# Performance work log

Hardware: AMD Instinct MI355X
Metric: run time of the kernel (lower is better)

The kernel has to match this reference:

```python
import jax, jax.numpy as jnp
import numpy as np

B, N, K = 8, 2048, 20
CIN, COUT, DIM, PH, MULT, UP = 256, 128, 64, 64, 4, 2
EPS = 1e-5

def _lin(k, o, i):
    return jax.random.normal(k, (o, i), jnp.float32) * (1.0 / np.sqrt(i))

def setup_inputs() -> dict:
    key = jax.random.key(0)
    ks = jax.random.split(key, 32)
    H = DIM * MULT
    return {
        'pos': jax.random.normal(ks[0], (B, 3, N), jnp.float32),
        'key_feat': jax.random.normal(ks[1], (B, CIN, N), jnp.float32),
        'query_feat': jax.random.normal(ks[2], (B, CIN, N), jnp.float32),
        'upfeat': jax.random.normal(ks[3], (B, CIN, N), jnp.float32),
        'mv_w1': _lin(ks[4], CIN, 2 * CIN), 'mv_b1': jnp.zeros(CIN),
        'mv_w2': _lin(ks[5], CIN, CIN), 'mv_b2': jnp.zeros(CIN),
        'mv_ws': _lin(ks[6], CIN, 2 * CIN), 'mv_bs': jnp.zeros(CIN),
        'wk': _lin(ks[7], DIM, CIN), 'bk': jnp.zeros(DIM),
        'wq': _lin(ks[8], DIM, CIN), 'bq': jnp.zeros(DIM),
        'wv': _lin(ks[9], DIM, CIN), 'bv': jnp.zeros(DIM),
        'wu': _lin(ks[10], DIM, CIN), 'bu': jnp.zeros(DIM),
        'pm_w1': _lin(ks[11], PH, 3), 'pm_b1': jnp.zeros(PH),
        'pm_g': jnp.ones(PH) + 0.1 * jax.random.normal(ks[12], (PH,)),
        'pm_be': 0.1 * jax.random.normal(ks[13], (PH,)),
        'pm_m': 0.1 * jax.random.normal(ks[14], (PH,)),
        'pm_v': jax.random.uniform(ks[15], (PH,), minval=0.5, maxval=1.5),
        'pm_w2': _lin(ks[16], DIM, PH), 'pm_b2': jnp.zeros(DIM),
        'am_w1': _lin(ks[17], H, DIM), 'am_b1': jnp.zeros(H),
        'am_g': jnp.ones(H) + 0.1 * jax.random.normal(ks[18], (H,)),
        'am_be': 0.1 * jax.random.normal(ks[19], (H,)),
        'am_m': 0.1 * jax.random.normal(ks[20], (H,)),
        'am_v': jax.random.uniform(ks[21], (H,), minval=0.5, maxval=1.5),
        'am_wt': jax.random.normal(ks[22], (H, DIM, UP), jnp.float32) * (1.0 / np.sqrt(H)),
        'am_bt': jnp.zeros(DIM),
        'we': _lin(ks[23], COUT, DIM), 'be': jnp.zeros(COUT),
        'wr': _lin(ks[24], COUT, CIN), 'br': jnp.zeros(COUT),
    }

def _c1(x, w, b):  # 1x1 Conv1d: x (B,C,N)
    return jnp.einsum('oc,bcn->bon', w, x) + b[None, :, None]

def _c2(x, w, b):  # 1x1 Conv2d: x (B,C,N,K)
    return jnp.einsum('oc,bcnk->bonk', w, x) + b[None, :, None, None]

def _bn(x, g, be, m, v):  # eval-mode BatchNorm2d over channel dim
    sc = g / jnp.sqrt(v + EPS)
    return x * sc[None, :, None, None] + (be - m * sc)[None, :, None, None]

def _group(f, idx):  # f (B,C,N), idx (B,N,K) -> (B,C,N,K)
    return jax.vmap(lambda fb, ib: fb[:, ib])(f, idx)

def reference(pos, key_feat, query_feat, upfeat, mv_w1, mv_b1, mv_w2, mv_b2, mv_ws, mv_bs, wk, bk, wq, bq, wv, bv, wu, bu, pm_w1, pm_b1, pm_g, pm_be, pm_m, pm_v, pm_w2, pm_b2, am_w1, am_b1, am_g, am_be, am_m, am_v, am_wt, am_bt, we, be, wr, br):
    # mlp_v: MLP_Res(in=2*CIN, hidden=CIN, out=CIN)
    x = jnp.concatenate([key_feat, query_feat], axis=1)
    value = _c1(jax.nn.relu(_c1(x, mv_w1, mv_b1)), mv_w2, mv_b2) + _c1(x, mv_ws, mv_bs)
    identity = value
    k = _c1(key_feat, wk, bk)
    q = _c1(query_feat, wq, bq)
    v = _c1(value, wv, bv)
    # self-KNN on pos
    pt = jnp.swapaxes(pos, 1, 2)  # (B,N,3)
    sq = jnp.sum(pt * pt, -1)
    d2 = sq[:, :, None] + sq[:, None, :] - 2.0 * jnp.einsum('bnc,bmc->bnm', pt, pt)
    _, idx = jax.lax.top_k(-d2, K)  # (B,N,K)
    k_g = _group(k, idx)
    qk_rel = q[..., None] - k_g  # (B,DIM,N,K)
    pos_rel = pos[..., None] - _group(pos, idx)  # (B,3,N,K)
    pe = _c2(jax.nn.relu(_bn(_c2(pos_rel, pm_w1, pm_b1), pm_g, pm_be, pm_m, pm_v)), pm_w2, pm_b2)
    uf = _c1(upfeat, wu, bu)
    uf_rel = uf[..., None] - _group(uf, idx)
    # attn_mlp: conv2d -> BN -> ReLU -> ConvTranspose2d((UP,1),(UP,1))
    h = jax.nn.relu(_bn(_c2(qk_rel + pe + uf_rel, am_w1, am_b1), am_g, am_be, am_m, am_v))  # (B,H,N,K)
    attn = jnp.einsum('bcnk,cor->bonrk', h, am_wt)  # (B,DIM,N,UP,K)
    b_, o_, n_, r_, k_ = attn.shape
    attn = attn.reshape(b_, o_, n_ * r_, k_) + am_bt[None, :, None, None]  # (B,DIM,UP*N,K)
    attn = jax.nn.softmax(attn, axis=-1)  # scale_layer = Softmax(dim=-1)
    val = _group(v, idx) + pe + uf_rel  # (B,DIM,N,K)
    val = jnp.repeat(val, UP, axis=2)  # nearest Upsample (UP,1)
    agg = jnp.sum(attn * val, axis=-1)  # (B,DIM,UP*N)
    y = _c1(agg, we, be)
    iden = jnp.repeat(_c1(identity, wr, br), UP, axis=2)
    return y + iden
```

## Files before the change

kernel.cpp:

```cpp
#include <hip/hip_runtime.h>
#include <hip/hip_bf16.h>

constexpr int B_ = 8, N_ = 2048, K_ = 20;
constexpr float EPS_ = 1e-5f;

constexpr int OW1P = 0;
constexpr int OWSP = OW1P + 256 * 256;
constexpr int OW2P = OWSP + 256 * 256;
constexpr int OWVP = OW2P + 128 * 256;
constexpr int OWRP = OWVP + 128 * 64;
constexpr int OWQT = OWRP + 128 * 128;
constexpr int OWKT = OWQT + 256 * 64;
constexpr int OWUT = OWKT + 256 * 64;
constexpr int OWET = OWUT + 256 * 64;
constexpr int OWTF = OWET + 64 * 128;
constexpr int OAWF = OWTF + 16384;
constexpr int OPWF = OAWF + 8192;
constexpr int OPW1 = OPWF + 2048;
constexpr int OB1  = OPW1 + 192;
constexpr int OBS2 = OB1 + 256;
constexpr int OBQ  = OBS2 + 256;
constexpr int OBK  = OBQ + 64;
constexpr int OBV  = OBK + 64;
constexpr int OBU  = OBV + 64;
constexpr int OBR  = OBU + 64;
constexpr int OBE  = OBR + 128;
constexpr int OPB1 = OBE + 128;
constexpr int OPSC = OPB1 + 64;
constexpr int OPSH = OPSC + 64;
constexpr int OPB2 = OPSH + 64;
constexpr int OASC = OPB2 + 64;
constexpr int OASH = OASC + 256;
constexpr int OAB1 = OASH + 256;
constexpr int OABT = OAB1 + 256;

constexpr size_t OFFB_WF   = 0;
constexpr size_t OFFB_IDX  = (size_t)2 << 20;
constexpr size_t OFFB_Q    = (size_t)4 << 20;
constexpr size_t OFFB_K    = (size_t)8 << 20;
constexpr size_t OFFB_U    = (size_t)12 << 20;
constexpr size_t OFFB_V    = (size_t)16 << 20;
constexpr size_t OFFB_IDEN = (size_t)20 << 20;

struct InPtrs { const float* p[38]; };

typedef _Float16 half2_t __attribute__((ext_vector_type(2)));
typedef _Float16 f16x8_t __attribute__((ext_vector_type(8)));
typedef float    f32x4_t __attribute__((ext_vector_type(4)));

union U4H8 { uint4 u; f16x8_t h; };

__device__ __forceinline__ unsigned pkh2(float a, float b) {
  union { unsigned u; half2_t h; } x;
  x.h = half2_t{(_Float16)a, (_Float16)b};
  return x.u;
}
__device__ __forceinline__ f32x4_t mfma_16x16x32(f16x8_t a, f16x8_t b, f32x4_t c) {
  return __builtin_amdgcn_mfma_f32_16x16x32_f16(a, b, c, 0, 0, 0);
}

__global__ __launch_bounds__(256) void k_prep(InPtrs in, float* __restrict__ wf) {
  const int tid = blockIdx.x * 256 + threadIdx.x;
  const int nth = gridDim.x * 256;
  const float *mv_w1 = in.p[4], *mv_b1 = in.p[5], *mv_w2 = in.p[6], *mv_b2 = in.p[7],
              *mv_ws = in.p[8], *mv_bs = in.p[9], *wk = in.p[10], *bk = in.p[11],
              *wq = in.p[12], *bq = in.p[13], *wv = in.p[14], *bv = in.p[15],
              *wu = in.p[16], *bu = in.p[17], *pm_w1 = in.p[18], *pm_b1 = in.p[19],
              *pm_g = in.p[20], *pm_be = in.p[21], *pm_m = in.p[22], *pm_v = in.p[23],
              *pm_w2 = in.p[24], *pm_b2 = in.p[25], *am_w1 = in.p[26], *am_b1 = in.p[27],
              *am_g = in.p[28], *am_be = in.p[29], *am_m = in.p[30], *am_v = in.p[31],
              *am_wt = in.p[32], *am_bt = in.p[33], *we = in.p[34], *be = in.p[35],
              *wr = in.p[36], *br = in.p[37];

  {
    unsigned* w1f = (unsigned*)(wf + OW1P);
    for (int i = tid; i < 65536; i += nth) {
      int q = i & 3, l = (i >> 2) & 63, ks = (i >> 8) & 15, mt = i >> 12;
      int m = mt * 16 + (l & 15);
      int k = ks * 32 + ((l >> 4) << 3) + 2 * q;
      w1f[i] = pkh2(mv_w1[m * 512 + k], mv_w1[m * 512 + k + 1]);
    }
    unsigned* wsf = (unsigned*)(wf + OWSP);
    for (int i = tid; i < 65536; i += nth) {
      int q = i & 3, l = (i >> 2) & 63, ks = (i >> 8) & 15, mt = i >> 12;
      int m = mt * 16 + (l & 15);
      int k = ks * 32 + ((l >> 4) << 3) + 2 * q;
      wsf[i] = pkh2(mv_ws[m * 512 + k], mv_ws[m * 512 + k + 1]);
    }
    unsigned* w2f = (unsigned*)(wf + OW2P);
    for (int i = tid; i < 32768; i += nth) {
      int q = i & 3, l = (i >> 2) & 63, ks = (i >> 8) & 7, mt = i >> 11;
      int m = mt * 16 + (l & 15);
      int k = ks * 32 + ((l >> 4) << 3) + 2 * q;
      w2f[i] = pkh2(mv_w2[m * 256 + k], mv_w2[m * 256 + k + 1]);
    }
    unsigned* wvf = (unsigned*)(wf + OWVP);
    for (int i = tid; i < 8192; i += nth) {
      int q = i & 3, l = (i >> 2) & 63, ks = (i >> 8) & 7, mt = i >> 11;
      int m = mt * 16 + (l & 15);
      int k = ks * 32 + ((l >> 4) << 3) + 2 * q;
      wvf[i] = pkh2(wv[m * 256 + k], wv[m * 256 + k + 1]);
    }
    unsigned* wrf = (unsigned*)(wf + OWRP);
    for (int i = tid; i < 16384; i += nth) {
      int q = i & 3, l = (i >> 2) & 63, ks = (i >> 8) & 7, mt = i >> 11;
      int m = mt * 16 + (l & 15);
      int k = ks * 32 + ((l >> 4) << 3) + 2 * q;
      wrf[i] = pkh2(wr[m * 256 + k], wr[m * 256 + k + 1]);
    }
    unsigned* wqf = (unsigned*)(wf + OWQT);
    for (int i = tid; i < 8192; i += nth) {
      int q = i & 3, l = (i >> 2) & 63, ks = (i >> 8) & 7, mt = i >> 11;
      int m = mt * 16 + (l & 15);
      int k = ks * 32 + ((l >> 4) << 3) + 2 * q;
      wqf[i] = pkh2(wq[m * 256 + k], wq[m * 256 + k + 1]);
    }
    unsigned* wkf = (unsigned*)(wf + OWKT);
    for (int i = tid; i < 8192; i += nth) {
      int q = i & 3, l = (i >> 2) & 63, ks = (i >> 8) & 7, mt = i >> 11;
      int m = mt * 16 + (l & 15);
      int k = ks * 32 + ((l >> 4) << 3) + 2 * q;
      wkf[i] = pkh2(wk[m * 256 + k], wk[m * 256 + k + 1]);
    }
  }
  for (int i = tid; i < 256 * 64; i += nth) { int c = i >> 6, m = i & 63; wf[OWUT + i] = wu[m * 256 + c]; }
  for (int i = tid; i < 64 * 128; i += nth) { int o = i >> 7, co = i & 127; wf[OWET + i] = we[co * 64 + o]; }

  {
    unsigned* wtf = (unsigned*)(wf + OWTF);
    for (int i = tid; i < 16384; i += nth) {
      int q = i & 3, l = (i >> 2) & 63, ks = (i >> 8) & 7, mt = i >> 11;
      int orr = mt * 16 + (l & 15);
      int c = ks * 32 + ((l >> 4) << 3) + 2 * q;
      wtf[i] = pkh2(am_wt[c * 128 + orr], am_wt[(c + 1) * 128 + orr]);
    }
  }
  {
    unsigned* awf = (unsigned*)(wf + OAWF);
    for (int i = tid; i < 8192; i += nth) {
      int q = i & 3, l = (i >> 2) & 63, ks = (i >> 8) & 1, mt = i >> 9;
      int c = mt * 16 + (l & 15);
      int o = ks * 32 + ((l >> 4) << 3) + 2 * q;
      awf[i] = pkh2(am_w1[c * 64 + o], am_w1[c * 64 + o + 1]);
    }
  }
  {
    unsigned* pwf = (unsigned*)(wf + OPWF);
    for (int i = tid; i < 2048; i += nth) {
      int q = i & 3, l = (i >> 2) & 63, ks = (i >> 8) & 1, mt = i >> 9;
      int o = mt * 16 + (l & 15);
      int ph = ks * 32 + ((l >> 4) << 3) + 2 * q;
      pwf[i] = pkh2(pm_w2[o * 64 + ph], pm_w2[o * 64 + ph + 1]);
    }
  }
  for (int i = tid; i < 192; i += nth) wf[OPW1 + i] = pm_w1[i];
  for (int i = tid; i < 256; i += nth) {
    wf[OB1 + i] = mv_b1[i];
    wf[OBS2 + i] = mv_bs[i] + mv_b2[i];
    float sc = am_g[i] / sqrtf(am_v[i] + EPS_);
    wf[OASC + i] = sc;
    wf[OASH + i] = am_be[i] - am_m[i] * sc;
    wf[OAB1 + i] = am_b1[i];
  }
  for (int i = tid; i < 64; i += nth) {
    wf[OBQ + i] = bq[i]; wf[OBK + i] = bk[i];
    wf[OBV + i] = bv[i]; wf[OBU + i] = bu[i];
    wf[OABT + i] = am_bt[i]; wf[OPB1 + i] = pm_b1[i]; wf[OPB2 + i] = pm_b2[i];
    float sc = pm_g[i] / sqrtf(pm_v[i] + EPS_);
    wf[OPSC + i] = sc;
    wf[OPSH + i] = pm_be[i] - pm_m[i] * sc;
  }
  for (int i = tid; i < 128; i += nth) { wf[OBR + i] = br[i]; wf[OBE + i] = be[i]; }
}

__global__ __launch_bounds__(256, 2) void k_mv(const float* __restrict__ wf,
                                               const float* __restrict__ keyf,
                                               const float* __restrict__ qryf,
                                               float* __restrict__ vout,
                                               float* __restrict__ idenout,
                                               float* __restrict__ qout,
                                               float* __restrict__ kout) {
  const int b = blockIdx.y;
  const int n0 = blockIdx.x * 32;
  const int tid = threadIdx.x, lane = tid & 63, wid = tid >> 6;
  __shared__ __align__(16) char smem[49152];
  char* xsb = smem;
  char* hbb = smem + 32768;
  char* vbb = smem;

  {
    const int col = tid & 31, kq = tid >> 5;
    const int swz = (col & 7) << 4;
#pragma unroll 4
    for (int it = 0; it < 32; ++it) {
      int k2 = it * 8 + kq;
      int c = 2 * k2;
      const float* s = (c < 256) ? keyf : qryf;
      size_t base = ((size_t)b * 256 + (c & 255)) * N_ + n0 + col;
      float x0 = s[base], x1 = s[base + N_];
      *(unsigned*)(xsb + ((col * 1024 + k2 * 4) ^ swz)) = pkh2(x0, x1);
    }
  }
  __syncthreads();

  f32x4_t acch[4][2], accs[4][2];
#pragma unroll
  for (int m = 0; m < 4; ++m)
#pragma unroll
    for (int nt = 0; nt < 2; ++nt) {
      acch[m][nt] = f32x4_t{0.f, 0.f, 0.f, 0.f};
      accs[m][nt] = f32x4_t{0.f, 0.f, 0.f, 0.f};
    }
  {
    const uint4* w1f = (const uint4*)((const unsigned*)(wf + OW1P));
    const uint4* wsf = (const uint4*)((const unsigned*)(wf + OWSP));
#pragma unroll 2
    for (int ks = 0; ks < 16; ++ks) {
      U4H8 bu[2];
#pragma unroll
      for (int nt = 0; nt < 2; ++nt) {
        int col = nt * 16 + (lane & 15);
        bu[nt].u = *(const uint4*)(xsb + ((col * 1024 + ks * 64 + ((lane >> 4) << 4)) ^ ((col & 7) << 4)));
      }
#pragma unroll
      for (int m = 0; m < 4; ++m) {
        U4H8 a1, as_;
        a1.u = w1f[((wid * 4 + m) * 16 + ks) * 64 + lane];
        as_.u = wsf[((wid * 4 + m) * 16 + ks) * 64 + lane];
#pragma unroll
        for (int nt = 0; nt < 2; ++nt) {
          acch[m][nt] = mfma_16x16x32(a1.h, bu[nt].h, acch[m][nt]);
          accs[m][nt] = mfma_16x16x32(as_.h, bu[nt].h, accs[m][nt]);
        }
      }
    }
  }
#pragma unroll
  for (int m = 0; m < 4; ++m) {
    int ch0 = (wid * 4 + m) * 16 + ((lane >> 4) << 2);
    float4 b1v = *(const float4*)(wf + OB1 + ch0);
#pragma unroll
    for (int nt = 0; nt < 2; ++nt) {
      int col = nt * 16 + (lane & 15);
      float h0 = fmaxf(acch[m][nt][0] + b1v.x, 0.f);
      float h1 = fmaxf(acch[m][nt][1] + b1v.y, 0.f);
      float h2 = fmaxf(acch[m][nt][2] + b1v.z, 0.f);
      float h3 = fmaxf(acch[m][nt][3] + b1v.w, 0.f);
      uint2 p;
      p.x = pkh2(h0, h1);
      p.y = pkh2(h2, h3);
      *(uint2*)(hbb + ((col * 512 + ch0 * 2) ^ ((col & 7) << 4))) = p;
    }
  }

  {
    f32x4_t accq[2], acck[2];
#pragma unroll
    for (int nt = 0; nt < 2; ++nt) {
      accq[nt] = f32x4_t{0.f, 0.f, 0.f, 0.f};
      acck[nt] = f32x4_t{0.f, 0.f, 0.f, 0.f};
    }
    const uint4* wqf = (const uint4*)((const unsigned*)(wf + OWQT));
    const uint4* wkf = (const uint4*)((const unsigned*)(wf + OWKT));
#pragma unroll 2
    for (int ks8 = 0; ks8 < 8; ++ks8) {
      U4H8 bk_[2], bq_[2];
#pragma unroll
      for (int nt = 0; nt < 2; ++nt) {
        int col = nt * 16 + (lane & 15);
        int swz = (col & 7) << 4;
        bk_[nt].u = *(const uint4*)(xsb + ((col * 1024 + ks8 * 64 + ((lane >> 4) << 4)) ^ swz));
        bq_[nt].u = *(const uint4*)(xsb + ((col * 1024 + (8 + ks8) * 64 + ((lane >> 4) << 4)) ^ swz));
      }
      U4H8 aq, ak;
      aq.u = wqf[(wid * 8 + ks8) * 64 + lane];
      ak.u = wkf[(wid * 8 + ks8) * 64 + lane];
#pragma unroll
      for (int nt = 0; nt < 2; ++nt) {
        acck[nt] = mfma_16x16x32(ak.h, bk_[nt].h, acck[nt]);
        accq[nt] = mfma_16x16x32(aq.h, bq_[nt].h, accq[nt]);
      }
    }
    int ch0 = wid * 16 + ((lane >> 4) << 2);
    float4 bqv = *(const float4*)(wf + OBQ + ch0);
    float4 bkv = *(const float4*)(wf + OBK + ch0);
#pragma unroll
    for (int nt = 0; nt < 2; ++nt) {
      int col = nt * 16 + (lane & 15);
      *(float4*)(qout + ((size_t)b * N_ + n0 + col) * 64 + ch0) =
          make_float4(accq[nt][0] + bqv.x, accq[nt][1] + bqv.y,
                      accq[nt][2] + bqv.z, accq[nt][3] + bqv.w);
      *(float4*)(kout + ((size_t)b * N_ + n0 + col) * 64 + ch0) =
          make_float4(acck[nt][0] + bkv.x, acck[nt][1] + bkv.y,
                      acck[nt][2] + bkv.z, acck[nt][3] + bkv.w);
    }
  }
  __syncthreads();

  {
    f32x4_t acc2[4][2];
#pragma unroll
    for (int m = 0; m < 4; ++m)
#pragma unroll
      for (int nt = 0; nt < 2; ++nt) acc2[m][nt] = f32x4_t{0.f, 0.f, 0.f, 0.f};
    const uint4* w2f = (const uint4*)((const unsigned*)(wf + OW2P));
#pragma unroll 2
    for (int ks = 0; ks < 8; ++ks) {
      U4H8 bu[2];
#pragma unroll
      for (int nt = 0; nt < 2; ++nt) {
        int col = nt * 16 + (lane & 15);
        bu[nt].u = *(const uint4*)(hbb + ((col * 512 + ks * 64 + ((lane >> 4) << 4)) ^ ((col & 7) << 4)));
      }
#pragma unroll
      for (int m = 0; m < 4; ++m) {
        U4H8 a2;
        a2.u = w2f[((wid * 4 + m) * 8 + ks) * 64 + lane];
#pragma unroll
        for (int nt = 0; nt < 2; ++nt)
          acc2[m][nt] = mfma_16x16x32(a2.h, bu[nt].h, acc2[m][nt]);
      }
    }
#pragma unroll
    for (int m = 0; m < 4; ++m) {
      int ch0 = (wid * 4 + m) * 16 + ((lane >> 4) << 2);
      float4 bsv = *(const float4*)(wf + OBS2 + ch0);
#pragma unroll
      for (int nt = 0; nt < 2; ++nt) {
        int col = nt * 16 + (lane & 15);
        float v0 = acc2[m][nt][0] + accs[m][nt][0] + bsv.x;
        float v1 = acc2[m][nt][1] + accs[m][nt][1] + bsv.y;
        float v2 = acc2[m][nt][2] + accs[m][nt][2] + bsv.z;
        float v3 = acc2[m][nt][3] + accs[m][nt][3] + bsv.w;
        uint2 p;
        p.x = pkh2(v0, v1);
        p.y = pkh2(v2, v3);
        *(uint2*)(vbb + ((col * 512 + ch0 * 2) ^ ((col & 7) << 4))) = p;
      }
    }
  }
  __syncthreads();

  {
    f32x4_t accv[2], accr[2][2];
#pragma unroll
    for (int nt = 0; nt < 2; ++nt) {
      accv[nt] = f32x4_t{0.f, 0.f, 0.f, 0.f};
      accr[0][nt] = f32x4_t{0.f, 0.f, 0.f, 0.f};
      accr[1][nt] = f32x4_t{0.f, 0.f, 0.f, 0.f};
    }
    const uint4* wvf = (const uint4*)((const unsigned*)(wf + OWVP));
    const uint4* wrf = (const uint4*)((const unsigned*)(wf + OWRP));
#pragma unroll 2
    for (int ks = 0; ks < 8; ++ks) {
      U4H8 bu[2];
#pragma unroll
      for (int nt = 0; nt < 2; ++nt) {
        int col = nt * 16 + (lane & 15);
        bu[nt].u = *(const uint4*)(vbb + ((col * 512 + ks * 64 + ((lane >> 4) << 4)) ^ ((col & 7) << 4)));
      }
      U4H8 av;
      av.u = wvf[(wid * 8 + ks) * 64 + lane];
#pragma unroll
      for (int nt = 0; nt < 2; ++nt)
        accv[nt] = mfma_16x16x32(av.h, bu[nt].h, accv[nt]);
#pragma unroll
      for (int m2 = 0; m2 < 2; ++m2) {
        U4H8 ar;
        ar.u = wrf[((wid * 2 + m2) * 8 + ks) * 64 + lane];
#pragma unroll
        for (int nt = 0; nt < 2; ++nt)
          accr[m2][nt] = mfma_16x16x32(ar.h, bu[nt].h, accr[m2][nt]);
      }
    }
    {
      int ch0 = wid * 16 + ((lane >> 4) << 2);
      float4 bvv = *(const float4*)(wf + OBV + ch0);
#pragma unroll
      for (int nt = 0; nt < 2; ++nt) {
        int col = nt * 16 + (lane & 15);
        *(float4*)(vout + ((size_t)b * N_ + n0 + col) * 64 + ch0) =
            make_float4(accv[nt][0] + bvv.x, accv[nt][1] + bvv.y,
                        accv[nt][2] + bvv.z, accv[nt][3] + bvv.w);
      }
    }
#pragma unroll
    for (int m2 = 0; m2 < 2; ++m2) {
      int ch0 = (wid * 2 + m2) * 16 + ((lane >> 4) << 2);
      float4 brv = *(const float4*)(wf + OBR + ch0);
#pragma unroll
      for (int nt = 0; nt < 2; ++nt) {
        int col = nt * 16 + (lane & 15);
        *(float4*)(idenout + ((size_t)b * N_ + n0 + col) * 128 + ch0) =
            make_float4(accr[m2][nt][0] + brv.x, accr[m2][nt][1] + brv.y,
                        accr[m2][nt][2] + brv.z, accr[m2][nt][3] + brv.w);
      }
    }
  }
}

__global__ __launch_bounds__(256) void k_gemm_u(const float* __restrict__ wf,
                                                const float* __restrict__ x,
                                                float* __restrict__ out) {
  const int b = blockIdx.y;
  const int n0 = blockIdx.x * 64;
  const float* Wt = wf + OWUT;
  const float* bias = wf + OBU;
  __shared__ float ws_[16][64];
  __shared__ float xs_[16][64];
  const int tid = threadIdx.x, tm = tid & 15, tn = tid >> 4;
  float acc[4][4] = {};
  for (int kt = 0; kt < 256; kt += 16) {
    for (int i = tid; i < 1024; i += 256) {
      int kk = i >> 6, col = i & 63;
      ws_[kk][col] = Wt[(size_t)(kt + kk) * 64 + col];
      xs_[kk][col] = x[((size_t)b * 256 + kt + kk) * N_ + n0 + col];
    }
    __syncthreads();
#pragma unroll
    for (int kk = 0; kk < 16; ++kk) {
      float4 x4 = *(const float4*)&xs_[kk][tn * 4];
      float4 w4 = *(const float4*)&ws_[kk][tm * 4];
      float wv[4] = {w4.x, w4.y, w4.z, w4.w};
      float xv[4] = {x4.x, x4.y, x4.z, x4.w};
#pragma unroll
      for (int i = 0; i < 4; ++i)
#pragma unroll
        for (int j = 0; j < 4; ++j) acc[i][j] += wv[i] * xv[j];
    }
    __syncthreads();
  }
#pragma unroll
  for (int j = 0; j < 4; ++j) {
    *(float4*)(out + ((size_t)b * N_ + n0 + tn * 4 + j) * 64 + tm * 4) =
        make_float4(acc[0][j] + bias[tm * 4], acc[1][j] + bias[tm * 4 + 1],
                    acc[2][j] + bias[tm * 4 + 2], acc[3][j] + bias[tm * 4 + 3]);
  }
}

__device__ __forceinline__ unsigned long long bitonic64_(unsigned long long v,
                                                         int lane) {
#pragma unroll
  for (int k = 2; k <= 64; k <<= 1) {
#pragma unroll
    for (int j = k >> 1; j > 0; j >>= 1) {
      unsigned long long o = (unsigned long long)__shfl_xor((long long)v, j);
      bool up = (lane & k) == 0;
      bool lower = (lane & j) == 0;
      bool keepmin = (lower == up);
      unsigned long long mn = o < v ? o : v;
      unsigned long long mx = o < v ? v : o;
      v = keepmin ? mn : mx;
    }
  }
  return v;
}

__global__ __launch_bounds__(256, 8) void k_knn(const float* __restrict__ pos,
                                                int* __restrict__ idxout) {
  const int b = blockIdx.x >> 11, n = blockIdx.x & 2047;
  __shared__ unsigned long long wkeys[4][20];
  __shared__ unsigned long long cand[4][64];
  const int tid = threadIdx.x;
  const int lane = tid & 63, wv = tid >> 6;
  const float* pb = pos + (size_t)b * 3 * N_;
  const double xq = pb[n], yq = pb[N_ + n], zq = pb[2 * N_ + n];
  const double sq = xq * xq + yq * yq + zq * zq;
  unsigned long long key[8];
#pragma unroll
  for (int s = 0; s < 8; ++s) {
    int i = tid + s * 256;
    double x = pb[i], y = pb[N_ + i], z = pb[2 * N_ + i];
    double psq = x * x + y * y + z * z;
    double dot = xq * x + yq * y + zq * z;
    double d2 = fmax((sq + psq) - 2.0 * dot, 0.0);
    key[s] = ((unsigned long long)__double_as_longlong(d2) & ~0x7FFull) |
             (unsigned long long)i;
  }
  unsigned long long m = key[0];
#pragma unroll
  for (int s = 1; s < 8; ++s) m = key[s] < m ? key[s] : m;

  unsigned long long v = bitonic64_(m, lane);
  unsigned long long T = (unsigned long long)__shfl((long long)v, 19);

  int c = 0;
#pragma unroll
  for (int s = 0; s < 8; ++s) c += (key[s] <= T) ? 1 : 0;
  int inc = c;
#pragma unroll
  for (int d = 1; d < 64; d <<= 1) {
    int t = __shfl_up(inc, d);
    if (lane >= d) inc += t;
  }
  const int C = __shfl(inc, 63);
  const int off = inc - c;

  if (C <= 64) {
    int o2 = off;
#pragma unroll
    for (int s = 0; s < 8; ++s) {
      if (key[s] <= T) { cand[wv][o2] = key[s]; ++o2; }
    }
    __builtin_amdgcn_wave_barrier();
    asm volatile("s_waitcnt lgkmcnt(0)" ::: "memory");
    unsigned long long cv = (lane < C) ? cand[wv][lane] : ~0ull;
    cv = bitonic64_(cv, lane);
    if (lane < K_) wkeys[wv][lane] = cv;
  } else {
    for (int r = 0; r < K_; ++r) {
      unsigned long long bk = key[0];
#pragma unroll
      for (int s = 1; s < 8; ++s) bk = key[s] < bk ? key[s] : bk;
      unsigned long long wk = bk;
#pragma unroll
      for (int mm = 32; mm; mm >>= 1) {
        unsigned long long ok = (unsigned long long)__shfl_xor((long long)wk, mm);
        if (ok < wk) wk = ok;
      }
      if (lane == 0) wkeys[wv][r] = wk;
      const int widx = (int)(wk & 0x7FF);
#pragma unroll
      for (int s = 0; s < 8; ++s)
        if (widx == tid + s * 256) key[s] = ~0ull;
    }
  }
  __syncthreads();

  if (tid < 128) {
    const int w = tid >> 5, p = tid & 31;
    if (p < 20) {
      const unsigned long long Kk = wkeys[w][p];
      int rank = p;
#pragma unroll
      for (int w2 = 0; w2 < 4; ++w2) {
        if (w2 == w) continue;
        int lo = 0, hi = 20;
        while (lo < hi) {
          int mid = (lo + hi) >> 1;
          if (wkeys[w2][mid] < Kk) lo = mid + 1; else hi = mid;
        }
        rank += lo;
      }
      if (rank < K_)
        idxout[((size_t)b * N_ + n) * K_ + rank] = (int)(Kk & 0x7FF);
    }
  }
}

__global__ __launch_bounds__(256, 4) void k_attn(
    const float* __restrict__ wf,
    const float* __restrict__ qb, const float* __restrict__ kb,
    const float* __restrict__ vb, const float* __restrict__ ub,
    const float* __restrict__ idenb, const int* __restrict__ idxb,
    const float* __restrict__ pos, float* __restrict__ out) {
  const int lb = ((int)blockIdx.x & 7) * 2048 + ((int)blockIdx.x >> 3);
  const int b = lb >> 11, n = lb & 2047;
  const int tid = threadIdx.x;
  const int lane = tid & 63, wid = tid >> 6;

  __shared__ __align__(16) char smem[26512];
  char*  Sb   = smem;
  char*  hb   = smem + 4096;
  char*  t1b  = smem + 4096;
  char*  peb  = smem + 8192;
  float* lg   = (float*)(smem + 4096);
  float* sVal = (float*)(smem + 20480);
  float* aggs = (float*)(smem + 25680);
  int*   idxs = (int*)(smem + 26192);
  float* prx  = (float*)(smem + 26272);
  float* pry  = (float*)(smem + 26352);
  float* prz  = (float*)(smem + 26432);

  if (tid < 20) idxs[tid] = idxb[((size_t)b * N_ + n) * K_ + tid] & 2047;
  __syncthreads();

  float sreg[5], vreg[5];
  {
    size_t rowq = ((size_t)b * N_ + n) * 64;
    float qvo = qb[rowq + lane];
    float ufo = ub[rowq + lane];
#pragma unroll
    for (int t = 0; t < 5; ++t) {
      int kk = wid * 5 + t;
      int j = idxs[kk];
      size_t rowj = ((size_t)b * N_ + j) * 64;
      float kvv = kb[rowj + lane], vvv = vb[rowj + lane], uvv = ub[rowj + lane];
      float ur = ufo - uvv;
      sreg[t] = (qvo - kvv) + ur;
      vreg[t] = vvv + ur;
    }
    if (tid < 20) {
      int j = idxs[tid];
      const float* pp = pos + (size_t)b * 3 * N_;
      prx[tid] = pp[n] - pp[j];
      pry[tid] = pp[N_ + n] - pp[N_ + j];
      prz[tid] = pp[2 * N_ + n] - pp[2 * N_ + j];
    }
  }
  __syncthreads();

  {
    int ph = lane;
    float w0 = wf[OPW1 + ph * 3], w1 = wf[OPW1 + ph * 3 + 1], w2 = wf[OPW1 + ph * 3 + 2];
    float pb1 = wf[OPB1 + ph], sc = wf[OPSC + ph], sh = wf[OPSH + ph];
#pragma unroll
    for (int t = 0; t < 5; ++t) {
      int kk = wid * 5 + t;
      float u = pb1 + w0 * prx[kk] + w1 * pry[kk] + w2 * prz[kk];
      float tv = fmaxf(u * sc + sh, 0.f);
      *(_Float16*)(t1b + ((kk * 128 + ph * 2) ^ ((kk & 7) << 4))) = (_Float16)tv;
    }
  }
  __syncthreads();

  {
    f32x4_t pacc[2];
#pragma unroll
    for (int nt = 0; nt < 2; ++nt) pacc[nt] = f32x4_t{0.f, 0.f, 0.f, 0.f};
    const int mt = wid;
#pragma unroll
    for (int ks = 0; ks < 2; ++ks) {
      U4H8 a;
      a.u = ((const uint4*)((const unsigned*)(wf + OPWF)))[(mt * 2 + ks) * 64 + lane];
#pragma unroll
      for (int nt = 0; nt < 2; ++nt) {
        int kc = nt * 16 + (lane & 15);
        U4H8 bu;
        bu.u = *(const uint4*)(t1b + ((kc * 128 + (ks * 32 + ((lane >> 4) << 3)) * 2) ^ ((kc & 7) << 4)));
        pacc[nt] = mfma_16x16x32(a.h, bu.h, pacc[nt]);
      }
    }
    const int o0 = mt * 16 + ((lane >> 4) << 2);
    float4 pb2v = *(const float4*)(wf + OPB2 + o0);
#pragma unroll
    for (int nt = 0; nt < 2; ++nt) {
      int kc = nt * 16 + (lane & 15);
      if (kc < 20) {
        float4 o;
        o.x = pacc[nt][0] + pb2v.x; o.y = pacc[nt][1] + pb2v.y;
        o.z = pacc[nt][2] + pb2v.z; o.w = pacc[nt][3] + pb2v.w;
        *(float4*)(peb + ((kc * 256 + o0 * 4) ^ ((kc & 7) << 4))) = o;
      }
    }
  }
  __syncthreads();

  {
#pragma unroll
    for (int t = 0; t < 5; ++t) {
      int kk = wid * 5 + t;
      float pe = *(const float*)(peb + ((kk * 256 + lane * 4) ^ ((kk & 7) << 4)));
      float sv = sreg[t] + pe;
      float vv = vreg[t] + pe;
      sVal[kk * 65 + lane] = vv;
      *(_Float16*)(Sb + ((kk * 128 + lane * 2) ^ ((kk & 7) << 4))) = (_Float16)sv;
    }
  }
  __syncthreads();

#pragma unroll
  for (int pass = 0; pass < 2; ++pass) {
    const int mt0 = wid * 4 + pass * 2;
    f32x4_t acc[2][2];
#pragma unroll
    for (int m = 0; m < 2; ++m)
#pragma unroll
      for (int nt = 0; nt < 2; ++nt) acc[m][nt] = f32x4_t{0.f, 0.f, 0.f, 0.f};
#pragma unroll
    for (int ks = 0; ks < 2; ++ks) {
      U4H8 bfr[2];
#pragma unroll
      for (int nt = 0; nt < 2; ++nt) {
        int kc = nt * 16 + (lane & 15);
        bfr[nt].u = *(const uint4*)(Sb + ((kc * 128 + (ks * 32 + ((lane >> 4) << 3)) * 2) ^ ((kc & 7) << 4)));
      }
#pragma unroll
      for (int m = 0; m < 2; ++m) {
        U4H8 a;
        a.u = ((const uint4*)((const unsigned*)(wf + OAWF)))[((mt0 + m) * 2 + ks) * 64 + lane];
#pragma unroll
        for (int nt = 0; nt < 2; ++nt)
          acc[m][nt] = mfma_16x16x32(a.h, bfr[nt].h, acc[m][nt]);
      }
    }
#pragma unroll
    for (int m = 0; m < 2; ++m) {
      const int c0 = (mt0 + m) * 16 + ((lane >> 4) << 2);
      float4 ab1 = *(const float4*)(wf + OAB1 + c0);
      float4 asc = *(const float4*)(wf + OASC + c0);
      float4 ash = *(const float4*)(wf + OASH + c0);
#pragma unroll
      for (int nt = 0; nt < 2; ++nt) {
        int kc = nt * 16 + (lane & 15);
        if (kc < 20) {
          float h0 = fmaxf((acc[m][nt][0] + ab1.x) * asc.x + ash.x, 0.f);
          float h1 = fmaxf((acc[m][nt][1] + ab1.y) * asc.y + ash.y, 0.f);
          float h2 = fmaxf((acc[m][nt][2] + ab1.z) * asc.z + ash.z, 0.f);
          float h3 = fmaxf((acc[m][nt][3] + ab1.w) * asc.w + ash.w, 0.f);
          uint2 p;
          p.x = pkh2(h0, h1);
          p.y = pkh2(h2, h3);
          *(uint2*)(hb + ((kc * 512 + c0 * 2) ^ ((kc & 7) << 4))) = p;
        }
      }
    }
  }
  __syncthreads();

  {
    f32x4_t acc5[2][2];
#pragma unroll
    for (int m = 0; m < 2; ++m)
#pragma unroll
      for (int nt = 0; nt < 2; ++nt) acc5[m][nt] = f32x4_t{0.f, 0.f, 0.f, 0.f};
#pragma unroll
    for (int ks = 0; ks < 8; ++ks) {
      U4H8 bfr[2];
#pragma unroll
      for (int nt = 0; nt < 2; ++nt) {
        int kc = nt * 16 + (lane & 15);
        bfr[nt].u = *(const uint4*)(hb + ((kc * 512 + (ks * 32 + ((lane >> 4) << 3)) * 2) ^ ((kc & 7) << 4)));
      }
#pragma unroll
      for (int m = 0; m < 2; ++m) {
        U4H8 a;
        a.u = ((const uint4*)((const unsigned*)(wf + OWTF)))[((wid * 2 + m) * 8 + ks) * 64 + lane];
#pragma unroll
        for (int nt = 0; nt < 2; ++nt)
          acc5[m][nt] = mfma_16x16x32(a.h, bfr[nt].h, acc5[m][nt]);
      }
    }
    __syncthreads();
#pragma unroll
    for (int m = 0; m < 2; ++m) {
      const int or0 = (wid * 2 + m) * 16 + ((lane >> 4) << 2);
#pragma unroll
      for (int nt = 0; nt < 2; ++nt) {
        int kc = nt * 16 + (lane & 15);
        if (kc < 20) {
#pragma unroll
          for (int r = 0; r < 4; ++r) lg[kc * 129 + or0 + r] = acc5[m][nt][r];
        }
      }
    }
  }
  __syncthreads();

  if (tid < 128) {
    int orr = tid, o = orr >> 1;
    float l[20];
#pragma unroll
    for (int kk = 0; kk < 20; ++kk) l[kk] = lg[kk * 129 + orr];
    float bt = wf[OABT + o];
    float m = -3.4e38f;
#pragma unroll
    for (int kk = 0; kk < 20; ++kk) { l[kk] += bt; m = fmaxf(m, l[kk]); }
    float s = 0.f;
#pragma unroll
    for (int kk = 0; kk < 20; ++kk) { l[kk] = expf(l[kk] - m); s += l[kk]; }
    float inv = 1.f / s;
    float a = 0.f;
#pragma unroll
    for (int kk = 0; kk < 20; ++kk) a += l[kk] * sVal[kk * 65 + o];
    aggs[orr] = a * inv;
  }
  __syncthreads();

  {
    int co = tid & 127, r = tid >> 7;
    float idv = idenb[((size_t)b * N_ + n) * 128 + co];
    float y = wf[OBE + co];
    const float* w = wf + OWET + co;
#pragma unroll 4
    for (int o = 0; o < 64; ++o) y += w[o * 128] * aggs[o * 2 + r];
    out[((size_t)b * 128 + co) * (size_t)(2 * N_) + 2 * n + r] = y + idv;
  }
}

extern "C" void kernel_launch(void* const* d_in, const int* in_sizes, int n_in,
                              void* d_out, int out_size, void* d_ws, size_t ws_size,
                              hipStream_t stream) {
  (void)in_sizes; (void)n_in; (void)out_size; (void)ws_size;
  InPtrs ip;
  for (int i = 0; i < 38; ++i) ip.p[i] = (const float*)d_in[i];
  char* ws = (char*)d_ws;
  float* wf    = (float*)(ws + OFFB_WF);
  int*   idxb  = (int*)(ws + OFFB_IDX);
  float* qb    = (float*)(ws + OFFB_Q);
  float* kb    = (float*)(ws + OFFB_K);
  float* ubuf  = (float*)(ws + OFFB_U);
  float* vbuf  = (float*)(ws + OFFB_V);
  float* idenb = (float*)(ws + OFFB_IDEN);

  k_prep<<<dim3(256), dim3(256), 0, stream>>>(ip, wf);
  k_mv<<<dim3(64, 8), dim3(256), 0, stream>>>(wf, ip.p[1], ip.p[2], vbuf, idenb, qb, kb);
  k_gemm_u<<<dim3(32, 8), dim3(256), 0, stream>>>(wf, ip.p[3], ubuf);
  k_knn<<<dim3(B_ * N_), dim3(256), 0, stream>>>(ip.p[0], idxb);
  k_attn<<<dim3(B_ * N_), dim3(256), 0, stream>>>(wf, qb, kb, vbuf, ubuf, idenb, idxb,
                                                  ip.p[0], (float*)d_out);
}
```

Baseline: 448.4 us.

## Process two query points per attention block to fill MFMA tiles

The attention kernel now handles two query points per block, packing 40 neighbor columns into three 16-wide MFMA N-tiles instead of 20 into two, so less of each tile is padding. Weight fragment loads are shared across both points, and all 256 threads do softmax work. The value buffer is stored as fp16, and the output projection weights are laid out row-major so they can be read as float4. The cost is more shared memory and registers per block, which may lower occupancy, plus some precision loss in the values.

```diff
diff --git a/kernel.cpp b/kernel.cpp
--- a/kernel.cpp
+++ b/kernel.cpp
@@ -124,7 +124,7 @@
     }
   }
   for (int i = tid; i < 256 * 64; i += nth) { int c = i >> 6, m = i & 63; wf[OWUT + i] = wu[m * 256 + c]; }
-  for (int i = tid; i < 64 * 128; i += nth) { int o = i >> 7, co = i & 127; wf[OWET + i] = we[co * 64 + o]; }
+  for (int i = tid; i < 64 * 128; i += nth) wf[OWET + i] = we[i];
 
   {
     unsigned* wtf = (unsigned*)(wf + OWTF);
@@ -554,48 +554,53 @@
     const float* __restrict__ vb, const float* __restrict__ ub,
     const float* __restrict__ idenb, const int* __restrict__ idxb,
     const float* __restrict__ pos, float* __restrict__ out) {
-  const int lb = ((int)blockIdx.x & 7) * 2048 + ((int)blockIdx.x >> 3);
-  const int b = lb >> 11, n = lb & 2047;
+  const int lb = ((int)blockIdx.x & 7) * 1024 + ((int)blockIdx.x >> 3);
+  const int b = lb >> 10, n0 = (lb & 1023) * 2;
   const int tid = threadIdx.x;
   const int lane = tid & 63, wid = tid >> 6;
 
-  __shared__ __align__(16) char smem[26512];
+  __shared__ __align__(16) char smem[38528];
   char*  Sb   = smem;
-  char*  hb   = smem + 4096;
-  char*  t1b  = smem + 4096;
-  char*  peb  = smem + 8192;
-  float* lg   = (float*)(smem + 4096);
-  float* sVal = (float*)(smem + 20480);
-  float* aggs = (float*)(smem + 25680);
-  int*   idxs = (int*)(smem + 26192);
-  float* prx  = (float*)(smem + 26272);
-  float* pry  = (float*)(smem + 26352);
-  float* prz  = (float*)(smem + 26432);
-
-  if (tid < 20) idxs[tid] = idxb[((size_t)b * N_ + n) * K_ + tid] & 2047;
-  __syncthreads();
-
-  float sreg[5], vreg[5];
-  {
-    size_t rowq = ((size_t)b * N_ + n) * 64;
+  char*  hb   = smem + 6144;
+  char*  t1b  = smem + 6144;
+  char*  peb  = smem + 12288;
+  float* lg   = (float*)(smem + 6144);
+  char*  svb  = smem + 30720;
+  float* aggs = (float*)(smem + 36864);
+  int*   idxs = (int*)(smem + 37888);
+  float* prx  = (float*)(smem + 38048);
+  float* pry  = (float*)(smem + 38208);
+  float* prz  = (float*)(smem + 38368);
+
+  if (tid < 40) {
+    int qi = tid >= 20;
+    idxs[tid] = idxb[((size_t)b * N_ + n0 + qi) * K_ + (tid - qi * 20)] & 2047;
+  }
+  __syncthreads();
+
+  float sreg[10], vreg[10];
+  {
+    const int qi = wid >> 1;
+    size_t rowq = ((size_t)b * N_ + n0 + qi) * 64;
     float qvo = qb[rowq + lane];
     float ufo = ub[rowq + lane];
 #pragma unroll
-    for (int t = 0; t < 5; ++t) {
-      int kk = wid * 5 + t;
-      int j = idxs[kk];
+    for (int t = 0; t < 10; ++t) {
+      int col = wid * 10 + t;
+      int j = idxs[col];
       size_t rowj = ((size_t)b * N_ + j) * 64;
       float kvv = kb[rowj + lane], vvv = vb[rowj + lane], uvv = ub[rowj + lane];
       float ur = ufo - uvv;
       sreg[t] = (qvo - kvv) + ur;
       vreg[t] = vvv + ur;
     }
-    if (tid < 20) {
+    if (tid < 40) {
       int j = idxs[tid];
+      int qn = n0 + (tid >= 20);
       const float* pp = pos + (size_t)b * 3 * N_;
-      prx[tid] = pp[n] - pp[j];
-      pry[tid] = pp[N_ + n] - pp[N_ + j];
-      prz[tid] = pp[2 * N_ + n] - pp[2 * N_ + j];
+      prx[tid] = pp[qn] - pp[j];
+      pry[tid] = pp[N_ + qn] - pp[N_ + j];
+      prz[tid] = pp[2 * N_ + qn] - pp[2 * N_ + j];
     }
   }
   __syncthreads();
@@ -605,26 +610,26 @@
     float w0 = wf[OPW1 + ph * 3], w1 = wf[OPW1 + ph * 3 + 1], w2 = wf[OPW1 + ph * 3 + 2];
     float pb1 = wf[OPB1 + ph], sc = wf[OPSC + ph], sh = wf[OPSH + ph];
 #pragma unroll
-    for (int t = 0; t < 5; ++t) {
-      int kk = wid * 5 + t;
-      float u = pb1 + w0 * prx[kk] + w1 * pry[kk] + w2 * prz[kk];
+    for (int t = 0; t < 10; ++t) {
+      int col = wid * 10 + t;
+      float u = pb1 + w0 * prx[col] + w1 * pry[col] + w2 * prz[col];
       float tv = fmaxf(u * sc + sh, 0.f);
-      *(_Float16*)(t1b + ((kk * 128 + ph * 2) ^ ((kk & 7) << 4))) = (_Float16)tv;
-    }
-  }
-  __syncthreads();
-
-  {
-    f32x4_t pacc[2];
-#pragma unroll
-    for (int nt = 0; nt < 2; ++nt) pacc[nt] = f32x4_t{0.f, 0.f, 0.f, 0.f};
+      *(_Float16*)(t1b + ((col * 128 + ph * 2) ^ ((col & 7) << 4))) = (_Float16)tv;
+    }
+  }
+  __syncthreads();
+
+  {
+    f32x4_t pacc[3];
+#pragma unroll
+    for (int nt = 0; nt < 3; ++nt) pacc[nt] = f32x4_t{0.f, 0.f, 0.f, 0.f};
     const int mt = wid;
 #pragma unroll
     for (int ks = 0; ks < 2; ++ks) {
       U4H8 a;
       a.u = ((const uint4*)((const unsigned*)(wf + OPWF)))[(mt * 2 + ks) * 64 + lane];
 #pragma unroll
-      for (int nt = 0; nt < 2; ++nt) {
+      for (int nt = 0; nt < 3; ++nt) {
         int kc = nt * 16 + (lane & 15);
         U4H8 bu;
         bu.u = *(const uint4*)(t1b + ((kc * 128 + (ks * 32 + ((lane >> 4) << 3)) * 2) ^ ((kc & 7) << 4)));
@@ -634,27 +639,25 @@
     const int o0 = mt * 16 + ((lane >> 4) << 2);
     float4 pb2v = *(const float4*)(wf + OPB2 + o0);
 #pragma unroll
-    for (int nt = 0; nt < 2; ++nt) {
+    for (int nt = 0; nt < 3; ++nt) {
       int kc = nt * 16 + (lane & 15);
-      if (kc < 20) {
-        float4 o;
-        o.x = pacc[nt][0] + pb2v.x; o.y = pacc[nt][1] + pb2v.y;
-        o.z = pacc[nt][2] + pb2v.z; o.w = pacc[nt][3] + pb2v.w;
-        *(float4*)(peb + ((kc * 256 + o0 * 4) ^ ((kc & 7) << 4))) = o;
-      }
-    }
-  }
-  __syncthreads();
-
-  {
-#pragma unroll
-    for (int t = 0; t < 5; ++t) {
-      int kk = wid * 5 + t;
-      float pe = *(const float*)(peb + ((kk * 256 + lane * 4) ^ ((kk & 7) << 4)));
+      float4 o;
+      o.x = pacc[nt][0] + pb2v.x; o.y = pacc[nt][1] + pb2v.y;
+      o.z = pacc[nt][2] + pb2v.z; o.w = pacc[nt][3] + pb2v.w;
+      *(float4*)(peb + ((kc * 256 + o0 * 4) ^ ((kc & 7) << 4))) = o;
+    }
+  }
+  __syncthreads();
+
+  {
+#pragma unroll
+    for (int t = 0; t < 10; ++t) {
+      int col = wid * 10 + t;
+      float pe = *(const float*)(peb + ((col * 256 + lane * 4) ^ ((col & 7) << 4)));
       float sv = sreg[t] + pe;
       float vv = vreg[t] + pe;
-      sVal[kk * 65 + lane] = vv;
-      *(_Float16*)(Sb + ((kk * 128 + lane * 2) ^ ((kk & 7) << 4))) = (_Float16)sv;
+      *(_Float16*)(svb + col * 128 + lane * 2) = (_Float16)vv;
+      *(_Float16*)(Sb + ((col * 128 + lane * 2) ^ ((col & 7) << 4))) = (_Float16)sv;
     }
   }
   __syncthreads();
@@ -662,16 +665,16 @@
 #pragma unroll
   for (int pass = 0; pass < 2; ++pass) {
     const int mt0 = wid * 4 + pass * 2;
-    f32x4_t acc[2][2];
+    f32x4_t acc[2][3];
 #pragma unroll
     for (int m = 0; m < 2; ++m)
 #pragma unroll
-      for (int nt = 0; nt < 2; ++nt) acc[m][nt] = f32x4_t{0.f, 0.f, 0.f, 0.f};
+      for (int nt = 0; nt < 3; ++nt) acc[m][nt] = f32x4_t{0.f, 0.f, 0.f, 0.f};
 #pragma unroll
     for (int ks = 0; ks < 2; ++ks) {
-      U4H8 bfr[2];
-#pragma unroll
-      for (int nt = 0; nt < 2; ++nt) {
+      U4H8 bfr[3];
+#pragma unroll
+      for (int nt = 0; nt < 3; ++nt) {
         int kc = nt * 16 + (lane & 15);
         bfr[nt].u = *(const uint4*)(Sb + ((kc * 128 + (ks * 32 + ((lane >> 4) << 3)) * 2) ^ ((kc & 7) << 4)));
       }
@@ -680,7 +683,7 @@
         U4H8 a;
         a.u = ((const uint4*)((const unsigned*)(wf + OAWF)))[((mt0 + m) * 2 + ks) * 64 + lane];
 #pragma unroll
-        for (int nt = 0; nt < 2; ++nt)
+        for (int nt = 0; nt < 3; ++nt)
           acc[m][nt] = mfma_16x16x32(a.h, bfr[nt].h, acc[m][nt]);
       }
     }
@@ -691,34 +694,32 @@
       float4 asc = *(const float4*)(wf + OASC + c0);
       float4 ash = *(const float4*)(wf + OASH + c0);
 #pragma unroll
-      for (int nt = 0; nt < 2; ++nt) {
+      for (int nt = 0; nt < 3; ++nt) {
         int kc = nt * 16 + (lane & 15);
-        if (kc < 20) {
-          float h0 = fmaxf((acc[m][nt][0] + ab1.x) * asc.x + ash.x, 0.f);
-          float h1 = fmaxf((acc[m][nt][1] + ab1.y) * asc.y + ash.y, 0.f);
-          float h2 = fmaxf((acc[m][nt][2] + ab1.z) * asc.z + ash.z, 0.f);
-          float h3 = fmaxf((acc[m][nt][3] + ab1.w) * asc.w + ash.w, 0.f);
-          uint2 p;
-          p.x = pkh2(h0, h1);
-          p.y = pkh2(h2, h3);
-          *(uint2*)(hb + ((kc * 512 + c0 * 2) ^ ((kc & 7) << 4))) = p;
-        }
-      }
-    }
-  }
-  __syncthreads();
-
-  {
-    f32x4_t acc5[2][2];
+        float h0 = fmaxf((acc[m][nt][0] + ab1.x) * asc.x + ash.x, 0.f);
+        float h1 = fmaxf((acc[m][nt][1] + ab1.y) * asc.y + ash.y, 0.f);
+        float h2 = fmaxf((acc[m][nt][2] + ab1.z) * asc.z + ash.z, 0.f);
+        float h3 = fmaxf((acc[m][nt][3] + ab1.w) * asc.w + ash.w, 0.f);
+        uint2 p;
+        p.x = pkh2(h0, h1);
+        p.y = pkh2(h2, h3);
+        *(uint2*)(hb + ((kc * 512 + c0 * 2) ^ ((kc & 7) << 4))) = p;
+      }
+    }
+  }
+  __syncthreads();
+
+  {
+    f32x4_t acc5[2][3];
 #pragma unroll
     for (int m = 0; m < 2; ++m)
 #pragma unroll
-      for (int nt = 0; nt < 2; ++nt) acc5[m][nt] = f32x4_t{0.f, 0.f, 0.f, 0.f};
+      for (int nt = 0; nt < 3; ++nt) acc5[m][nt] = f32x4_t{0.f, 0.f, 0.f, 0.f};
 #pragma unroll
     for (int ks = 0; ks < 8; ++ks) {
-      U4H8 bfr[2];
-#pragma unroll
-      for (int nt = 0; nt < 2; ++nt) {
+      U4H8 bfr[3];
+#pragma unroll
+      for (int nt = 0; nt < 3; ++nt) {
         int kc = nt * 16 + (lane & 15);
         bfr[nt].u = *(const uint4*)(hb + ((kc * 512 + (ks * 32 + ((lane >> 4) << 3)) * 2) ^ ((kc & 7) << 4)));
       }
@@ -727,7 +728,7 @@
         U4H8 a;
         a.u = ((const uint4*)((const unsigned*)(wf + OWTF)))[((wid * 2 + m) * 8 + ks) * 64 + lane];
 #pragma unroll
-        for (int nt = 0; nt < 2; ++nt)
+        for (int nt = 0; nt < 3; ++nt)
           acc5[m][nt] = mfma_16x16x32(a.h, bfr[nt].h, acc5[m][nt]);
       }
     }
@@ -736,9 +737,9 @@
     for (int m = 0; m < 2; ++m) {
       const int or0 = (wid * 2 + m) * 16 + ((lane >> 4) << 2);
 #pragma unroll
-      for (int nt = 0; nt < 2; ++nt) {
+      for (int nt = 0; nt < 3; ++nt) {
         int kc = nt * 16 + (lane & 15);
-        if (kc < 20) {
+        if (kc < 40) {
 #pragma unroll
           for (int r = 0; r < 4; ++r) lg[kc * 129 + or0 + r] = acc5[m][nt][r];
         }
@@ -747,11 +748,11 @@
   }
   __syncthreads();
 
-  if (tid < 128) {
-    int orr = tid, o = orr >> 1;
+  {
+    const int qsel = tid >> 7, orr = tid & 127, o = orr >> 1;
     float l[20];
 #pragma unroll
-    for (int kk = 0; kk < 20; ++kk) l[kk] = lg[kk * 129 + orr];
+    for (int kk = 0; kk < 20; ++kk) l[kk] = lg[(qsel * 20 + kk) * 129 + orr];
     float bt = wf[OABT + o];
     float m = -3.4e38f;
 #pragma unroll
@@ -762,19 +763,32 @@
     float inv = 1.f / s;
     float a = 0.f;
 #pragma unroll
-    for (int kk = 0; kk < 20; ++kk) a += l[kk] * sVal[kk * 65 + o];
-    aggs[orr] = a * inv;
-  }
-  __syncthreads();
-
-  {
-    int co = tid & 127, r = tid >> 7;
-    float idv = idenb[((size_t)b * N_ + n) * 128 + co];
-    float y = wf[OBE + co];
-    const float* w = wf + OWET + co;
+    for (int kk = 0; kk < 20; ++kk)
+      a += l[kk] * (float)(*(const _Float16*)(svb + (qsel * 20 + kk) * 128 + o * 2));
+    aggs[qsel * 128 + orr] = a * inv;
+  }
+  __syncthreads();
+
+  {
+    const int co = tid & 127, r = tid >> 7;
+    float y0 = wf[OBE + co], y1 = y0;
+    const float* w = wf + OWET + co * 64;
 #pragma unroll 4
-    for (int o = 0; o < 64; ++o) y += w[o * 128] * aggs[o * 2 + r];
-    out[((size_t)b * 128 + co) * (size_t)(2 * N_) + 2 * n + r] = y + idv;
+    for (int o4 = 0; o4 < 16; ++o4) {
+      float4 w4 = *(const float4*)(w + o4 * 4);
+      const float wv[4] = {w4.x, w4.y, w4.z, w4.w};
+#pragma unroll
+      for (int j = 0; j < 4; ++j) {
+        int oi = o4 * 4 + j;
+        y0 += wv[j] * aggs[oi * 2 + r];
+        y1 += wv[j] * aggs[128 + oi * 2 + r];
+      }
+    }
+    float id0 = idenb[((size_t)b * N_ + n0) * 128 + co];
+    float id1 = idenb[((size_t)b * N_ + n0 + 1) * 128 + co];
+    size_t obase = ((size_t)b * 128 + co) * (size_t)(2 * N_);
+    out[obase + 2 * n0 + r] = y0 + id0;
+    out[obase + 2 * n0 + 2 + r] = y1 + id1;
   }
 }
 
@@ -797,6 +811,6 @@
   k_mv<<<dim3(64, 8), dim3(256), 0, stream>>>(wf, ip.p[1], ip.p[2], vbuf, idenb, qb, kb);
   k_gemm_u<<<dim3(32, 8), dim3(256), 0, stream>>>(wf, ip.p[3], ubuf);
   k_knn<<<dim3(B_ * N_), dim3(256), 0, stream>>>(ip.p[0], idxb);
-  k_attn<<<dim3(B_ * N_), dim3(256), 0, stream>>>(wf, qb, kb, vbuf, ubuf, idenb, idxb,
-                                                  ip.p[0], (float*)d_out);
+  k_attn<<<dim3(B_ * N_ / 2), dim3(256), 0, stream>>>(wf, qb, kb, vbuf, ubuf, idenb, idxb,
+                                                      ip.p[0], (float*)d_out);
 }
```

Result: faster. 436.9 us (-2.6%).
